# Optimization experiments

Hardware: AMD Instinct MI355X
Metric: run time of the kernel (lower is better)

The kernel has to match this reference:

```python
import jax, jax.numpy as jnp
import numpy as np
import math

NUM_HEADS = 8
HEAD_DIM = 16  # hidden_features 128 / 8 heads
SCALE = 1.0 / math.sqrt(HEAD_DIM)


def setup_inputs() -> dict:
    key = jax.random.key(0)
    ks = jax.random.split(key, 9)
    N, E, F = 50000, 640000, 128
    node_h = jax.random.normal(ks[0], (N, F), jnp.float32)
    edge_h = jax.random.normal(ks[1], (E, F), jnp.float32)
    # distances kept strictly positive so distance**lambda (and its grad) is well-defined
    distance = jax.random.uniform(ks[2], (E, 1), jnp.float32, minval=0.1, maxval=1.0)
    src = jax.random.randint(ks[3], (E,), 0, N, jnp.int32)
    dst = jax.random.randint(ks[4], (E,), 0, N, jnp.int32)

    def lin(k):
        kw, kb = jax.random.split(k)
        W = jax.random.normal(kw, (F, F), jnp.float32) / math.sqrt(F)
        b = jax.random.normal(kb, (F,), jnp.float32) * 0.02
        return W, b

    Wq, bq = lin(ks[5])
    Wk, bk = lin(ks[6])
    Wv, bv = lin(ks[7])
    Wo, bo = lin(ks[8])
    lam = jnp.array(1.0, jnp.float32)  # attenuation_lambda (clamp in original is a no-op)
    return dict(node_h=node_h, edge_h=edge_h, distance=distance,
                Wq=Wq, bq=bq, Wk=Wk, bk=bk, Wv=Wv, bv=bv, Wo=Wo, bo=bo,
                lam=lam, src=src, dst=dst)


def _segment_softmax(logits, seg, num):
    # softmax over edges sharing the same destination node (DGL mailbox dim=1)
    m = jax.ops.segment_max(logits, seg, num_segments=num)
    m = jax.lax.stop_gradient(jnp.where(jnp.isfinite(m), m, 0.0))
    e = jnp.exp(logits - m[seg])
    den = jax.ops.segment_sum(e, seg, num_segments=num)
    den = jnp.where(den == 0, 1.0, den)  # guard zero in-degree nodes
    return e / den[seg]


def reference(node_h, edge_h, distance, Wq, bq, Wk, bk, Wv, bv, Wo, bo, lam, src, dst):
    N = node_h.shape[0]
    q = (node_h @ Wq.T + bq).reshape(N, NUM_HEADS, HEAD_DIM)
    k = (edge_h @ Wk.T + bk).reshape(-1, NUM_HEADS, HEAD_DIM)
    v = (node_h @ Wv.T + bv).reshape(N, NUM_HEADS, HEAD_DIM)
    qs, qd = q[src], q[dst]                      # [E, H, d] gathers
    in_m = jnp.sum(qs * k, axis=-1)              # [E, H]
    out_m = jnp.sum(qd * k, axis=-1)             # [E, H]
    diag_m = jnp.sum(qs * qd, axis=-1)           # [E, H]
    att = jnp.power(distance, lam)               # [E, 1] power-law attenuation
    score = (_segment_softmax(in_m * SCALE, dst, N)
             + _segment_softmax(out_m * SCALE, dst, N)
             + _segment_softmax(diag_m * SCALE, dst, N)) * att  # [E, H]
    # message value is edges.dst['v'] (as in the original), scatter-sum to dst
    h = jax.ops.segment_sum(score[..., None] * v[dst], dst, num_segments=N)
    h = h.reshape(N, NUM_HEADS * HEAD_DIM)
    out = h @ Wo.T + bo
    return jax.nn.leaky_relu(out, negative_slope=0.1)  # dropout is identity in eval
```

## Files before the change

### kernel.cpp

```cpp
#include <hip/hip_runtime.h>
#include <math.h>

#define H 8
#define FD 128
#define SCALE 0.25f

typedef __attribute__((ext_vector_type(8))) short bf16x8;
typedef __attribute__((ext_vector_type(4))) float f32x4;

__device__ __forceinline__ unsigned short bf_rne(float f) {
    unsigned u = __float_as_uint(f);
    u += 0x7FFFu + ((u >> 16) & 1u);
    return (unsigned short)(u >> 16);
}
__device__ __forceinline__ float bf_to_f(unsigned short s) {
    return __uint_as_float(((unsigned)s) << 16);
}
__device__ __forceinline__ bf16x8 cvt8(const float* __restrict__ p) {
    float4 a = *(const float4*)p;
    float4 b = *(const float4*)(p + 4);
    bf16x8 r;
    r[0] = bf_rne(a.x); r[1] = bf_rne(a.y); r[2] = bf_rne(a.z); r[3] = bf_rne(a.w);
    r[4] = bf_rne(b.x); r[5] = bf_rne(b.y); r[6] = bf_rne(b.z); r[7] = bf_rne(b.w);
    return r;
}

__global__ __launch_bounds__(256) void prep_kernel(
    const float* __restrict__ Wq, const float* __restrict__ Wk,
    const float* __restrict__ Wv, const float* __restrict__ Wo,
    unsigned short* __restrict__ oq, unsigned short* __restrict__ ok,
    unsigned short* __restrict__ ov, unsigned short* __restrict__ oo) {
    int i = blockIdx.x * 256 + threadIdx.x;
    const float* src[4] = {Wq, Wk, Wv, Wo};
    unsigned short* dstp[4] = {oq, ok, ov, oo};
#pragma unroll
    for (int m = 0; m < 4; ++m) {
        float4 w = ((const float4*)src[m])[i];
        ushort4 p = make_ushort4(bf_rne(w.x), bf_rne(w.y), bf_rne(w.z), bf_rne(w.w));
        *(ushort4*)(dstp[m] + i * 4) = p;
    }
}

__global__ __launch_bounds__(256) void qv_kernel(
    const float* __restrict__ X, const unsigned short* __restrict__ Wqb,
    const unsigned short* __restrict__ Wvb, const float* __restrict__ bq,
    const float* __restrict__ bv, unsigned short* __restrict__ qb,
    float* __restrict__ v, int Nrows) {
    const int t = threadIdx.x;
    const int lane = t & 63, wid = t >> 6;
    const int lm = lane & 15, lq = lane >> 4;
    const int r0 = blockIdx.x * 64 + wid * 16;

    bf16x8 a[4];
#pragma unroll
    for (int s = 0; s < 4; ++s) {
        int r = r0 + lm;
        if (r >= Nrows) r = Nrows - 1;
        a[s] = cvt8(X + (size_t)r * FD + s * 32 + lq * 8);
    }
#pragma unroll
    for (int g = 0; g < 2; ++g) {
        const unsigned short* Wb = g ? Wvb : Wqb;
        const float* bias = g ? bv : bq;
        f32x4 acc[8];
#pragma unroll
        for (int nt = 0; nt < 8; ++nt) {
            float b = bias[nt * 16 + lm];
            acc[nt][0] = b; acc[nt][1] = b; acc[nt][2] = b; acc[nt][3] = b;
        }
#pragma unroll
        for (int s = 0; s < 4; ++s)
#pragma unroll
            for (int nt = 0; nt < 8; ++nt) {
                bf16x8 bf = *(const bf16x8*)(Wb + (nt * 16 + lm) * FD + s * 32 + lq * 8);
                acc[nt] = __builtin_amdgcn_mfma_f32_16x16x32_bf16(
                    a[s], bf, acc[nt], 0, 0, 0);
            }
#pragma unroll
        for (int nt = 0; nt < 8; ++nt)
#pragma unroll
            for (int r = 0; r < 4; ++r) {
                int row = r0 + lq * 4 + r;
                if (row >= Nrows) continue;
                int col = nt * 16 + lm;
                if (g == 0)
                    qb[(size_t)row * FD + col] = bf_rne(acc[nt][r]);
                else
                    v[(size_t)row * FD + col] = acc[nt][r];
            }
    }
}

__global__ __launch_bounds__(256) void hist_kernel(
    const int* __restrict__ dst, int* __restrict__ cnt, int E) {
    int i = blockIdx.x * 256 + threadIdx.x;
    if (i < E) atomicAdd(cnt + dst[i], 1);
}

__global__ __launch_bounds__(256) void scan1_kernel(
    const int* __restrict__ cnt, int* __restrict__ offs,
    int* __restrict__ bsum, int N) {
    __shared__ int sd[256];
    int t = threadIdx.x, i = blockIdx.x * 256 + t;
    int x = (i < N) ? cnt[i] : 0;
    int v = x;
    sd[t] = v; __syncthreads();
#pragma unroll
    for (int off = 1; off < 256; off <<= 1) {
        int y = (t >= off) ? sd[t - off] : 0;
        __syncthreads();
        v += y; sd[t] = v; __syncthreads();
    }
    if (i < N) offs[i] = v - x;
    if (t == 255) bsum[blockIdx.x] = v;
}

__global__ __launch_bounds__(256) void scan2_kernel(int* __restrict__ bsum, int NB) {
    __shared__ int sd[256];
    int t = threadIdx.x;
    int x = (t < NB) ? bsum[t] : 0;
    int v = x;
    sd[t] = v; __syncthreads();
#pragma unroll
    for (int off = 1; off < 256; off <<= 1) {
        int y = (t >= off) ? sd[t - off] : 0;
        __syncthreads();
        v += y; sd[t] = v; __syncthreads();
    }
    if (t < NB) bsum[t] = v - x;
}

__global__ __launch_bounds__(256) void scan3_kernel(
    int* __restrict__ offs, int* __restrict__ cursor,
    const int* __restrict__ bsum, int N, int E) {
    int i = blockIdx.x * 256 + threadIdx.x;
    if (i < N) {
        int o = offs[i] + bsum[blockIdx.x];
        offs[i] = o;
        cursor[i] = o;
    }
    if (i == 0) offs[N] = E;
}

__global__ __launch_bounds__(256) void scatter_kernel(
    const int* __restrict__ src, const int* __restrict__ dst,
    const float* __restrict__ distance, const float* __restrict__ lam,
    int* __restrict__ cursor, int* __restrict__ rank,
    int* __restrict__ srcs_s, float* __restrict__ att_s, int E) {
    int i = blockIdx.x * 256 + threadIdx.x;
    if (i >= E) return;
    int d = dst[i];
    int r = atomicAdd(cursor + d, 1);
    rank[i] = r;
    srcs_s[r] = src[i];
    att_s[r] = __expf(lam[0] * __logf(distance[i]));
}

__global__ __launch_bounds__(256) void kproj_sorted_kernel(
    const float* __restrict__ X, const unsigned short* __restrict__ Wkb,
    const float* __restrict__ bk, const int* __restrict__ rank,
    unsigned short* __restrict__ kb, int E) {
    const int t = threadIdx.x;
    const int lane = t & 63, wid = t >> 6;
    const int lm = lane & 15, lq = lane >> 4;
    const int r0 = blockIdx.x * 64 + wid * 16;

    bf16x8 a[4];
#pragma unroll
    for (int s = 0; s < 4; ++s) {
        int r = r0 + lm;
        if (r >= E) r = E - 1;
        a[s] = cvt8(X + (size_t)r * FD + s * 32 + lq * 8);
    }
    f32x4 acc[8];
#pragma unroll
    for (int nt = 0; nt < 8; ++nt) {
        float b = bk[nt * 16 + lm];
        acc[nt][0] = b; acc[nt][1] = b; acc[nt][2] = b; acc[nt][3] = b;
    }
#pragma unroll
    for (int s = 0; s < 4; ++s)
#pragma unroll
        for (int nt = 0; nt < 8; ++nt) {
            bf16x8 bf = *(const bf16x8*)(Wkb + (nt * 16 + lm) * FD + s * 32 + lq * 8);
            acc[nt] = __builtin_amdgcn_mfma_f32_16x16x32_bf16(
                a[s], bf, acc[nt], 0, 0, 0);
        }
#pragma unroll
    for (int r = 0; r < 4; ++r) {
        int e = r0 + lq * 4 + r;
        if (e >= E) continue;
        int rk = rank[e];
        unsigned short* dstrow = kb + (size_t)rk * FD + lm;
#pragma unroll
        for (int nt = 0; nt < 8; ++nt)
            dstrow[nt * 16] = bf_rne(acc[nt][r]);
    }
}

__global__ __launch_bounds__(256) void seg_attn_kernel(
    const unsigned short* __restrict__ kb, const unsigned short* __restrict__ qb,
    const int* __restrict__ offs, const int* __restrict__ srcs_s,
    const float* __restrict__ att_s, float* __restrict__ ssum, int NH) {
    int i = blockIdx.x * 256 + threadIdx.x;
    if (i >= NH) return;
    int n = i >> 3, h = i & 7;
    int s0 = offs[n], s1 = offs[n + 1];

    const unsigned short* qdp = qb + (size_t)n * FD + h * 16;
    bf16x8 qd0 = *(const bf16x8*)qdp;
    bf16x8 qd1 = *(const bf16x8*)(qdp + 8);

    float den1 = 0.f, den2 = 0.f, den3 = 0.f;
    float a1 = 0.f, a2 = 0.f, a3 = 0.f;
    for (int j = s0; j < s1; ++j) {
        const unsigned short* kp = kb + (size_t)j * FD + h * 16;
        bf16x8 k0 = *(const bf16x8*)kp;
        bf16x8 k1 = *(const bf16x8*)(kp + 8);
        int s = srcs_s[j];
        const unsigned short* qsp = qb + (size_t)s * FD + h * 16;
        bf16x8 qs0 = *(const bf16x8*)qsp;
        bf16x8 qs1 = *(const bf16x8*)(qsp + 8);
        float att = att_s[j];
        float pin = 0.f, pot = 0.f, pdg = 0.f;
#pragma unroll
        for (int q = 0; q < 8; ++q) {
            float qsf = bf_to_f((unsigned short)qs0[q]);
            float qdf = bf_to_f((unsigned short)qd0[q]);
            float kf  = bf_to_f((unsigned short)k0[q]);
            pin += qsf * kf; pot += qdf * kf; pdg += qsf * qdf;
        }
#pragma unroll
        for (int q = 0; q < 8; ++q) {
            float qsf = bf_to_f((unsigned short)qs1[q]);
            float qdf = bf_to_f((unsigned short)qd1[q]);
            float kf  = bf_to_f((unsigned short)k1[q]);
            pin += qsf * kf; pot += qdf * kf; pdg += qsf * qdf;
        }
        float e1 = __expf(pin * SCALE);
        float e2 = __expf(pot * SCALE);
        float e3 = __expf(pdg * SCALE);
        den1 += e1; a1 += e1 * att;
        den2 += e2; a2 += e2 * att;
        den3 += e3; a3 += e3 * att;
    }
    float r = 0.f;
    if (den1 != 0.f) r += a1 / den1;
    if (den2 != 0.f) r += a2 / den2;
    if (den3 != 0.f) r += a3 / den3;
    ssum[i] = r;
}

__global__ __launch_bounds__(256) void edge_kernel(
    const float* __restrict__ eh, const unsigned short* __restrict__ Wkb,
    const float* __restrict__ bk, const unsigned short* __restrict__ qb,
    const int* __restrict__ src, const int* __restrict__ dst,
    const float* __restrict__ distance, const float* __restrict__ lam,
    float* __restrict__ den1, float* __restrict__ den2,
    float* __restrict__ den3, float* __restrict__ sc1,
    float* __restrict__ sc2, float* __restrict__ sc3, int E) {
    __shared__ unsigned short lK[64 * 128];
    const int t = threadIdx.x;
    const int e0 = blockIdx.x * 64;
    const int lane = t & 63, wid = t >> 6;
    const int lm = lane & 15, lq = lane >> 4;
    const int wm = wid * 16;

    bf16x8 a[4];
#pragma unroll
    for (int s = 0; s < 4; ++s) {
        int e = e0 + wm + lm;
        if (e >= E) e = E - 1;
        a[s] = cvt8(eh + (size_t)e * FD + s * 32 + lq * 8);
    }
    f32x4 acc[8];
#pragma unroll
    for (int nt = 0; nt < 8; ++nt) {
        float b = bk[nt * 16 + lm];
        acc[nt][0] = b; acc[nt][1] = b; acc[nt][2] = b; acc[nt][3] = b;
    }
#pragma unroll
    for (int s = 0; s < 4; ++s)
#pragma unroll
        for (int nt = 0; nt < 8; ++nt) {
            bf16x8 bf = *(const bf16x8*)(Wkb + (nt * 16 + lm) * FD + s * 32 + lq * 8);
            acc[nt] = __builtin_amdgcn_mfma_f32_16x16x32_bf16(
                a[s], bf, acc[nt], 0, 0, 0);
        }
#pragma unroll
    for (int nt = 0; nt < 8; ++nt)
#pragma unroll
        for (int r = 0; r < 4; ++r) {
            int m = wm + lq * 4 + r;
            int n = nt * 16 + lm;
            int swb = (n >> 3) ^ (m & 7);
            lK[m * 128 + swb * 8 + (n & 7)] = bf_rne(acc[nt][r]);
        }
    __syncthreads();

    const float lamv = lam[0];
#pragma unroll
    for (int i = 0; i < 2; ++i) {
        int p = i * 256 + t;
        int el = p >> 3, h = p & 7;
        int e = e0 + el;
        if (e >= E) continue;
        int si = src[e], di = dst[e];
        const unsigned short* qsp = qb + (size_t)si * FD + h * 16;
        const unsigned short* qdp = qb + (size_t)di * FD + h * 16;
        bf16x8 qs0 = *(const bf16x8*)qsp;
        bf16x8 qs1 = *(const bf16x8*)(qsp + 8);
        bf16x8 qd0 = *(const bf16x8*)qdp;
        bf16x8 qd1 = *(const bf16x8*)(qdp + 8);
        int swb0 = (2 * h) ^ (el & 7), swb1 = (2 * h + 1) ^ (el & 7);
        bf16x8 k0 = *(const bf16x8*)(lK + el * 128 + swb0 * 8);
        bf16x8 k1 = *(const bf16x8*)(lK + el * 128 + swb1 * 8);
        float pin = 0.f, pot = 0.f, pdg = 0.f;
#pragma unroll
        for (int j = 0; j < 8; ++j) {
            float qsf = bf_to_f((unsigned short)qs0[j]);
            float qdf = bf_to_f((unsigned short)qd0[j]);
            float kf = bf_to_f((unsigned short)k0[j]);
            pin += qsf * kf; pot += qdf * kf; pdg += qsf * qdf;
        }
#pragma unroll
        for (int j = 0; j < 8; ++j) {
            float qsf = bf_to_f((unsigned short)qs1[j]);
            float qdf = bf_to_f((unsigned short)qd1[j]);
            float kf = bf_to_f((unsigned short)k1[j]);
            pin += qsf * kf; pot += qdf * kf; pdg += qsf * qdf;
        }
        float att = __expf(lamv * __logf(distance[e]));
        float e1 = __expf(pin * SCALE);
        float e2 = __expf(pot * SCALE);
        float e3 = __expf(pdg * SCALE);
        int nb = di * H + h;
        atomicAdd(den1 + nb, e1); atomicAdd(sc1 + nb, e1 * att);
        atomicAdd(den2 + nb, e2); atomicAdd(sc2 + nb, e2 * att);
        atomicAdd(den3 + nb, e3); atomicAdd(sc3 + nb, e3 * att);
    }
}

__global__ __launch_bounds__(256) void combine_kernel(
    const float* __restrict__ den1, const float* __restrict__ den2,
    const float* __restrict__ den3, const float* __restrict__ sc1,
    const float* __restrict__ sc2, const float* __restrict__ sc3,
    float* __restrict__ ssum, int NH) {
    int i = blockIdx.x * 256 + threadIdx.x;
    if (i >= NH) return;
    float r = 0.f;
    float d1 = den1[i]; if (d1 != 0.f) r += sc1[i] / d1;
    float d2 = den2[i]; if (d2 != 0.f) r += sc2[i] / d2;
    float d3 = den3[i]; if (d3 != 0.f) r += sc3[i] / d3;
    ssum[i] = r;
}

__global__ __launch_bounds__(256) void out_kernel(
    const float* __restrict__ v, const float* __restrict__ ssum,
    const unsigned short* __restrict__ Wob, const float* __restrict__ bo,
    float* __restrict__ out, int Nrows) {
    const int t = threadIdx.x;
    const int lane = t & 63, wid = t >> 6;
    const int lm = lane & 15, lq = lane >> 4;
    const int r0 = blockIdx.x * 64 + wid * 16;

    bf16x8 a[4];
#pragma unroll
    for (int s = 0; s < 4; ++s) {
        int r = r0 + lm;
        if (r >= Nrows) r = Nrows - 1;
        int k0 = s * 32 + lq * 8;
        float sc = ssum[r * H + (k0 >> 4)];
        const float* p = v + (size_t)r * FD + k0;
        float4 x = *(const float4*)p;
        float4 y = *(const float4*)(p + 4);
        bf16x8 f;
        f[0] = bf_rne(x.x * sc); f[1] = bf_rne(x.y * sc);
        f[2] = bf_rne(x.z * sc); f[3] = bf_rne(x.w * sc);
        f[4] = bf_rne(y.x * sc); f[5] = bf_rne(y.y * sc);
        f[6] = bf_rne(y.z * sc); f[7] = bf_rne(y.w * sc);
        a[s] = f;
    }
    f32x4 acc[8];
#pragma unroll
    for (int nt = 0; nt < 8; ++nt) {
        float b = bo[nt * 16 + lm];
        acc[nt][0] = b; acc[nt][1] = b; acc[nt][2] = b; acc[nt][3] = b;
    }
#pragma unroll
    for (int s = 0; s < 4; ++s)
#pragma unroll
        for (int nt = 0; nt < 8; ++nt) {
            bf16x8 bf = *(const bf16x8*)(Wob + (nt * 16 + lm) * FD + s * 32 + lq * 8);
            acc[nt] = __builtin_amdgcn_mfma_f32_16x16x32_bf16(
                a[s], bf, acc[nt], 0, 0, 0);
        }
#pragma unroll
    for (int nt = 0; nt < 8; ++nt)
#pragma unroll
        for (int r = 0; r < 4; ++r) {
            int row = r0 + lq * 4 + r;
            if (row >= Nrows) continue;
            int col = nt * 16 + lm;
            float x = acc[nt][r];
            out[(size_t)row * FD + col] = x > 0.f ? x : 0.1f * x;
        }
}

extern "C" void kernel_launch(void* const* d_in, const int* in_sizes, int n_in,
                              void* d_out, int out_size, void* d_ws,
                              size_t ws_size, hipStream_t stream) {
    (void)n_in; (void)out_size;
    const float* node_h   = (const float*)d_in[0];
    const float* edge_h   = (const float*)d_in[1];
    const float* distance = (const float*)d_in[2];
    const float* Wq = (const float*)d_in[3];
    const float* bq = (const float*)d_in[4];
    const float* Wk = (const float*)d_in[5];
    const float* bk = (const float*)d_in[6];
    const float* Wv = (const float*)d_in[7];
    const float* bv = (const float*)d_in[8];
    const float* Wo = (const float*)d_in[9];
    const float* bo = (const float*)d_in[10];
    const float* lam = (const float*)d_in[11];
    const int* src = (const int*)d_in[12];
    const int* dst = (const int*)d_in[13];

    int N = in_sizes[0] / FD;
    int E = in_sizes[1] / FD;
    int NH = N * H;
    int NB = (N + 255) / 256;

    char* p = (char*)d_ws;
    auto alloc = [&](size_t bytes) -> char* {
        char* r = p;
        p += (bytes + 255) & ~(size_t)255;
        return r;
    };
    unsigned short* Wqb = (unsigned short*)alloc(FD * FD * 2);
    unsigned short* Wkb = (unsigned short*)alloc(FD * FD * 2);
    unsigned short* Wvb = (unsigned short*)alloc(FD * FD * 2);
    unsigned short* Wob = (unsigned short*)alloc(FD * FD * 2);
    unsigned short* qb  = (unsigned short*)alloc((size_t)N * FD * 2);
    float* v    = (float*)alloc((size_t)N * FD * 4);
    float* ssum = (float*)alloc((size_t)NH * 4);
    char* branch_base = p;

    int* cnt    = (int*)alloc((size_t)N * 4);
    int* offs   = (int*)alloc((size_t)(N + 1) * 4);
    int* cursor = (int*)alloc((size_t)N * 4);
    int* bsum   = (int*)alloc((size_t)NB * 4);
    int* rank   = (int*)alloc((size_t)E * 4);
    int* srcs_s = (int*)alloc((size_t)E * 4);
    float* att_s = (float*)alloc((size_t)E * 4);
    unsigned short* kb = (unsigned short*)alloc((size_t)E * FD * 2);
    size_t need_main = (size_t)(p - (char*)d_ws);

    bool main_ok = (ws_size >= need_main) && (NB <= 256);

    prep_kernel<<<16, 256, 0, stream>>>(Wq, Wk, Wv, Wo, Wqb, Wkb, Wvb, Wob);

    int nb = (N + 63) / 64;
    qv_kernel<<<nb, 256, 0, stream>>>(node_h, Wqb, Wvb, bq, bv, qb, v, N);

    if (main_ok) {
        hipMemsetAsync(cnt, 0, (size_t)N * 4, stream);
        int eb = (E + 255) / 256;
        hist_kernel<<<eb, 256, 0, stream>>>(dst, cnt, E);
        scan1_kernel<<<NB, 256, 0, stream>>>(cnt, offs, bsum, N);
        scan2_kernel<<<1, 256, 0, stream>>>(bsum, NB);
        scan3_kernel<<<NB, 256, 0, stream>>>(offs, cursor, bsum, N, E);
        scatter_kernel<<<eb, 256, 0, stream>>>(src, dst, distance, lam,
                                               cursor, rank, srcs_s, att_s, E);
        kproj_sorted_kernel<<<(E + 63) / 64, 256, 0, stream>>>(
            edge_h, Wkb, bk, rank, kb, E);
        seg_attn_kernel<<<(NH + 255) / 256, 256, 0, stream>>>(
            kb, qb, offs, srcs_s, att_s, ssum, NH);
    } else {
        char* q = branch_base;
        auto alloc2 = [&](size_t bytes) -> char* {
            char* r = q;
            q += (bytes + 255) & ~(size_t)255;
            return r;
        };
        float* den1 = (float*)alloc2((size_t)NH * 4);
        float* den2 = (float*)alloc2((size_t)NH * 4);
        float* den3 = (float*)alloc2((size_t)NH * 4);
        float* sc1  = (float*)alloc2((size_t)NH * 4);
        float* sc2  = (float*)alloc2((size_t)NH * 4);
        float* sc3  = (float*)alloc2((size_t)NH * 4);
        hipMemsetAsync(den1, 0, (size_t)(q - (char*)den1), stream);
        int ebl = (E + 63) / 64;
        edge_kernel<<<ebl, 256, 0, stream>>>(edge_h, Wkb, bk, qb, src, dst,
                                             distance, lam,
                                             den1, den2, den3, sc1, sc2, sc3, E);
        combine_kernel<<<(NH + 255) / 256, 256, 0, stream>>>(
            den1, den2, den3, sc1, sc2, sc3, ssum, NH);
    }

    out_kernel<<<nb, 256, 0, stream>>>(v, ssum, Wob, bo, (float*)d_out, N);
}
```

Measured before the change: 822.6 us.

## Swap MFMA operands for row-contiguous vector stores; split segment attention across 4 lanes

The three GEMM kernels now pass the weight tile as the A operand and activations as B, so each lane holds four consecutive output columns of one row. Each lane can then write a ushort4/float4 per tile instead of scattered scalar stores, which matters most for the rank-permuted k writes. The segment attention kernel assigns four lanes per (node, head) that stride over incoming edges and combine their partial sums with shuffles. This exposes more parallelism and memory-level concurrency for per-segment loops averaging about 13 edges, at the cost of quadruple the thread count and some redundant qd loads.

Measured after the change: 808.0 us. Within noise of the previous version (-1.8%).

```diff
diff --git a/kernel.cpp b/kernel.cpp
--- a/kernel.cpp
+++ b/kernel.cpp
@@ -50,14 +50,14 @@
     const int lane = t & 63, wid = t >> 6;
     const int lm = lane & 15, lq = lane >> 4;
     const int r0 = blockIdx.x * 64 + wid * 16;
-
-    bf16x8 a[4];
-#pragma unroll
-    for (int s = 0; s < 4; ++s) {
-        int r = r0 + lm;
-        if (r >= Nrows) r = Nrows - 1;
-        a[s] = cvt8(X + (size_t)r * FD + s * 32 + lq * 8);
-    }
+    const int er = r0 + lm;
+    const int erc = er < Nrows ? er : Nrows - 1;
+
+    bf16x8 x[4];
+#pragma unroll
+    for (int s = 0; s < 4; ++s)
+        x[s] = cvt8(X + (size_t)erc * FD + s * 32 + lq * 8);
+
 #pragma unroll
     for (int g = 0; g < 2; ++g) {
         const unsigned short* Wb = g ? Wvb : Wqb;
@@ -65,29 +65,37 @@
         f32x4 acc[8];
 #pragma unroll
         for (int nt = 0; nt < 8; ++nt) {
-            float b = bias[nt * 16 + lm];
-            acc[nt][0] = b; acc[nt][1] = b; acc[nt][2] = b; acc[nt][3] = b;
+            float4 bb = *(const float4*)(bias + nt * 16 + lq * 4);
+            acc[nt][0] = bb.x; acc[nt][1] = bb.y;
+            acc[nt][2] = bb.z; acc[nt][3] = bb.w;
         }
 #pragma unroll
         for (int s = 0; s < 4; ++s)
 #pragma unroll
             for (int nt = 0; nt < 8; ++nt) {
-                bf16x8 bf = *(const bf16x8*)(Wb + (nt * 16 + lm) * FD + s * 32 + lq * 8);
+                bf16x8 w = *(const bf16x8*)(Wb + (nt * 16 + lm) * FD + s * 32 + lq * 8);
                 acc[nt] = __builtin_amdgcn_mfma_f32_16x16x32_bf16(
-                    a[s], bf, acc[nt], 0, 0, 0);
+                    w, x[s], acc[nt], 0, 0, 0);
             }
-#pragma unroll
-        for (int nt = 0; nt < 8; ++nt)
-#pragma unroll
-            for (int r = 0; r < 4; ++r) {
-                int row = r0 + lq * 4 + r;
-                if (row >= Nrows) continue;
-                int col = nt * 16 + lm;
-                if (g == 0)
-                    qb[(size_t)row * FD + col] = bf_rne(acc[nt][r]);
-                else
-                    v[(size_t)row * FD + col] = acc[nt][r];
+        if (er < Nrows) {
+            if (g == 0) {
+                unsigned short* dr = qb + (size_t)er * FD;
+#pragma unroll
+                for (int nt = 0; nt < 8; ++nt) {
+                    ushort4 u = make_ushort4(bf_rne(acc[nt][0]), bf_rne(acc[nt][1]),
+                                             bf_rne(acc[nt][2]), bf_rne(acc[nt][3]));
+                    *(ushort4*)(dr + nt * 16 + lq * 4) = u;
+                }
+            } else {
+                float* dr = v + (size_t)er * FD;
+#pragma unroll
+                for (int nt = 0; nt < 8; ++nt) {
+                    float4 u = make_float4(acc[nt][0], acc[nt][1],
+                                           acc[nt][2], acc[nt][3]);
+                    *(float4*)(dr + nt * 16 + lq * 4) = u;
+                }
             }
+        }
     }
 }
 
@@ -164,37 +172,38 @@
     const int lane = t & 63, wid = t >> 6;
     const int lm = lane & 15, lq = lane >> 4;
     const int r0 = blockIdx.x * 64 + wid * 16;
-
-    bf16x8 a[4];
-#pragma unroll
-    for (int s = 0; s < 4; ++s) {
-        int r = r0 + lm;
-        if (r >= E) r = E - 1;
-        a[s] = cvt8(X + (size_t)r * FD + s * 32 + lq * 8);
-    }
+    const int er = r0 + lm;
+    const int erc = er < E ? er : E - 1;
+
+    bf16x8 x[4];
+#pragma unroll
+    for (int s = 0; s < 4; ++s)
+        x[s] = cvt8(X + (size_t)erc * FD + s * 32 + lq * 8);
+
     f32x4 acc[8];
 #pragma unroll
     for (int nt = 0; nt < 8; ++nt) {
-        float b = bk[nt * 16 + lm];
-        acc[nt][0] = b; acc[nt][1] = b; acc[nt][2] = b; acc[nt][3] = b;
+        float4 bb = *(const float4*)(bk + nt * 16 + lq * 4);
+        acc[nt][0] = bb.x; acc[nt][1] = bb.y;
+        acc[nt][2] = bb.z; acc[nt][3] = bb.w;
     }
 #pragma unroll
     for (int s = 0; s < 4; ++s)
 #pragma unroll
         for (int nt = 0; nt < 8; ++nt) {
-            bf16x8 bf = *(const bf16x8*)(Wkb + (nt * 16 + lm) * FD + s * 32 + lq * 8);
+            bf16x8 w = *(const bf16x8*)(Wkb + (nt * 16 + lm) * FD + s * 32 + lq * 8);
             acc[nt] = __builtin_amdgcn_mfma_f32_16x16x32_bf16(
-                a[s], bf, acc[nt], 0, 0, 0);
-        }
-#pragma unroll
-    for (int r = 0; r < 4; ++r) {
-        int e = r0 + lq * 4 + r;
-        if (e >= E) continue;
-        int rk = rank[e];
-        unsigned short* dstrow = kb + (size_t)rk * FD + lm;
-#pragma unroll
-        for (int nt = 0; nt < 8; ++nt)
-            dstrow[nt * 16] = bf_rne(acc[nt][r]);
+                w, x[s], acc[nt], 0, 0, 0);
+        }
+    if (er < E) {
+        int rk = rank[er];
+        unsigned short* dr = kb + (size_t)rk * FD;
+#pragma unroll
+        for (int nt = 0; nt < 8; ++nt) {
+            ushort4 u = make_ushort4(bf_rne(acc[nt][0]), bf_rne(acc[nt][1]),
+                                     bf_rne(acc[nt][2]), bf_rne(acc[nt][3]));
+            *(ushort4*)(dr + nt * 16 + lq * 4) = u;
+        }
     }
 }
 
@@ -202,9 +211,10 @@
     const unsigned short* __restrict__ kb, const unsigned short* __restrict__ qb,
     const int* __restrict__ offs, const int* __restrict__ srcs_s,
     const float* __restrict__ att_s, float* __restrict__ ssum, int NH) {
-    int i = blockIdx.x * 256 + threadIdx.x;
-    if (i >= NH) return;
-    int n = i >> 3, h = i & 7;
+    int tid = blockIdx.x * 256 + threadIdx.x;
+    int g = tid >> 2, slot = tid & 3;
+    if (g >= NH) return;
+    int n = g >> 3, h = g & 7;
     int s0 = offs[n], s1 = offs[n + 1];
 
     const unsigned short* qdp = qb + (size_t)n * FD + h * 16;
@@ -213,7 +223,7 @@
 
     float den1 = 0.f, den2 = 0.f, den3 = 0.f;
     float a1 = 0.f, a2 = 0.f, a3 = 0.f;
-    for (int j = s0; j < s1; ++j) {
+    for (int j = s0 + slot; j < s1; j += 4) {
         const unsigned short* kp = kb + (size_t)j * FD + h * 16;
         bf16x8 k0 = *(const bf16x8*)kp;
         bf16x8 k1 = *(const bf16x8*)(kp + 8);
@@ -244,11 +254,19 @@
         den2 += e2; a2 += e2 * att;
         den3 += e3; a3 += e3 * att;
     }
-    float r = 0.f;
-    if (den1 != 0.f) r += a1 / den1;
-    if (den2 != 0.f) r += a2 / den2;
-    if (den3 != 0.f) r += a3 / den3;
-    ssum[i] = r;
+#pragma unroll
+    for (int m = 1; m <= 2; m <<= 1) {
+        den1 += __shfl_xor(den1, m); a1 += __shfl_xor(a1, m);
+        den2 += __shfl_xor(den2, m); a2 += __shfl_xor(a2, m);
+        den3 += __shfl_xor(den3, m); a3 += __shfl_xor(a3, m);
+    }
+    if (slot == 0) {
+        float r = 0.f;
+        if (den1 != 0.f) r += a1 / den1;
+        if (den2 != 0.f) r += a2 / den2;
+        if (den3 != 0.f) r += a3 / den3;
+        ssum[g] = r;
+    }
 }
 
 __global__ __launch_bounds__(256) void edge_kernel(
@@ -363,48 +381,51 @@
     const int lane = t & 63, wid = t >> 6;
     const int lm = lane & 15, lq = lane >> 4;
     const int r0 = blockIdx.x * 64 + wid * 16;
-
-    bf16x8 a[4];
+    const int er = r0 + lm;
+    const int erc = er < Nrows ? er : Nrows - 1;
+
+    bf16x8 x[4];
 #pragma unroll
     for (int s = 0; s < 4; ++s) {
-        int r = r0 + lm;
-        if (r >= Nrows) r = Nrows - 1;
         int k0 = s * 32 + lq * 8;
-        float sc = ssum[r * H + (k0 >> 4)];
-        const float* p = v + (size_t)r * FD + k0;
-        float4 x = *(const float4*)p;
-        float4 y = *(const float4*)(p + 4);
+        float sc = ssum[erc * H + (k0 >> 4)];
+        const float* p = v + (size_t)erc * FD + k0;
+        float4 xa = *(const float4*)p;
+        float4 ya = *(const float4*)(p + 4);
         bf16x8 f;
-        f[0] = bf_rne(x.x * sc); f[1] = bf_rne(x.y * sc);
-        f[2] = bf_rne(x.z * sc); f[3] = bf_rne(x.w * sc);
-        f[4] = bf_rne(y.x * sc); f[5] = bf_rne(y.y * sc);
-        f[6] = bf_rne(y.z * sc); f[7] = bf_rne(y.w * sc);
-        a[s] = f;
+        f[0] = bf_rne(xa.x * sc); f[1] = bf_rne(xa.y * sc);
+        f[2] = bf_rne(xa.z * sc); f[3] = bf_rne(xa.w * sc);
+        f[4] = bf_rne(ya.x * sc); f[5] = bf_rne(ya.y * sc);
+        f[6] = bf_rne(ya.z * sc); f[7] = bf_rne(ya.w * sc);
+        x[s] = f;
     }
     f32x4 acc[8];
 #pragma unroll
     for (int nt = 0; nt < 8; ++nt) {
-        float b = bo[nt * 16 + lm];
-        acc[nt][0] = b; acc[nt][1] = b; acc[nt][2] = b; acc[nt][3] = b;
+        float4 bb = *(const float4*)(bo + nt * 16 + lq * 4);
+        acc[nt][0] = bb.x; acc[nt][1] = bb.y;
+        acc[nt][2] = bb.z; acc[nt][3] = bb.w;
     }
 #pragma unroll
     for (int s = 0; s < 4; ++s)
 #pragma unroll
         for (int nt = 0; nt < 8; ++nt) {
-            bf16x8 bf = *(const bf16x8*)(Wob + (nt * 16 + lm) * FD + s * 32 + lq * 8);
+            bf16x8 w = *(const bf16x8*)(Wob + (nt * 16 + lm) * FD + s * 32 + lq * 8);
             acc[nt] = __builtin_amdgcn_mfma_f32_16x16x32_bf16(
-                a[s], bf, acc[nt], 0, 0, 0);
-        }
-#pragma unroll
-    for (int nt = 0; nt < 8; ++nt)
-#pragma unroll
-        for (int r = 0; r < 4; ++r) {
-            int row = r0 + lq * 4 + r;
-            if (row >= Nrows) continue;
-            int col = nt * 16 + lm;
-            float x = acc[nt][r];
-            out[(size_t)row * FD + col] = x > 0.f ? x : 0.1f * x;
-        }
+                w, x[s], acc[nt], 0, 0, 0);
+        }
+    if (er < Nrows) {
+        float* dr = out + (size_t)er * FD;
+#pragma unroll
+        for (int nt = 0; nt < 8; ++nt) {
+            float4 u;
+            u.x = acc[nt][0] > 0.f ? acc[nt][0] : 0.1f * acc[nt][0];
+            u.y = acc[nt][1] > 0.f ? acc[nt][1] : 0.1f * acc[nt][1];
+            u.z = acc[nt][2] > 0.f ? acc[nt][2] : 0.1f * acc[nt][2];
+            u.w = acc[nt][3] > 0.f ? acc[nt][3] : 0.1f * acc[nt][3];
+            *(float4*)(dr + nt * 16 + lq * 4) = u;
+        }
+    }
 }
 
 extern "C" void kernel_launch(void* const* d_in, const int* in_sizes, int n_in,
@@ -474,7 +495,7 @@
                                                cursor, rank, srcs_s, att_s, E);
         kproj_sorted_kernel<<<(E + 63) / 64, 256, 0, stream>>>(
             edge_h, Wkb, bk, rank, kb, E);
-        seg_attn_kernel<<<(NH + 255) / 256, 256, 0, stream>>>(
+        seg_attn_kernel<<<(NH * 4 + 255) / 256, 256, 0, stream>>>(
             kb, qb, offs, srcs_s, att_s, ssum, NH);
     } else {
         char* q = branch_base;
```
